# Performance work log

Hardware: AMD Instinct MI355X
Metric: run time of the kernel (lower is better)

The kernel has to match this reference:

```python
import jax, jax.numpy as jnp
import numpy as np

B = 4096
INPUT_SIZE = 1000
HIDDEN = 512
NUM_MASKS = 4
GROUP_SIZE = 100  # int(1000 * 0.1)
NUM_GROUPS = INPUT_SIZE // GROUP_SIZE  # 10, divides evenly


def entmax(alpha, v):
    # matches the torch helper: softmax-like with alpha-power denominator
    v = v - jnp.max(v, axis=-1, keepdims=True)
    e = jnp.exp(v)
    s = (jnp.sum(e ** alpha, axis=-1, keepdims=True) + 1e-5) ** (1.0 / alpha)
    return e / s


def layernorm(h, w, b):
    # h: [..., H]; w,b broadcast to [..., H]
    mu = jnp.mean(h, axis=-1, keepdims=True)
    var = jnp.mean((h - mu) ** 2, axis=-1, keepdims=True)
    return (h - mu) * jax.lax.rsqrt(var + 1e-5) * w + b


def setup_inputs() -> dict:
    key = jax.random.key(0)
    ks = jax.random.split(key, 4)
    x = jax.random.normal(ks[0], (B, INPUT_SIZE), dtype=jnp.float32)
    W_masks = jax.random.normal(ks[1], (NUM_GROUPS, NUM_MASKS, GROUP_SIZE), dtype=jnp.float32)
    W1 = jax.random.normal(ks[2], (NUM_GROUPS, HIDDEN, GROUP_SIZE), dtype=jnp.float32)
    W2 = jax.random.normal(ks[3], (NUM_GROUPS, HIDDEN, GROUP_SIZE), dtype=jnp.float32)
    ln1_w = jnp.ones((NUM_GROUPS, HIDDEN), dtype=jnp.float32)
    ln1_b = jnp.zeros((NUM_GROUPS, HIDDEN), dtype=jnp.float32)
    ln2_w = jnp.ones((NUM_GROUPS, HIDDEN), dtype=jnp.float32)
    ln2_b = jnp.zeros((NUM_GROUPS, HIDDEN), dtype=jnp.float32)
    return {"x": x, "W_masks": W_masks, "W1": W1, "W2": W2,
            "ln1_w": ln1_w, "ln1_b": ln1_b, "ln2_w": ln2_w, "ln2_b": ln2_b}


def reference(x, W_masks, W1, W2, ln1_w, ln1_b, ln2_w, ln2_b):
    G, M, S = W_masks.shape
    b = x.shape[0]
    xg = x.reshape(b, G, S)                                  # [B,G,S]
    mask = entmax(1.1, W_masks)                              # [G,M,S]
    weighted = xg[:, :, None, :] * mask[None]                # [B,G,M,S]
    h1 = jnp.einsum('bgms,ghs->bgmh', weighted, W1)          # [B,G,M,H]
    h2 = jnp.einsum('bgms,ghs->bgmh', weighted, W2)
    n1 = layernorm(h1, ln1_w[None, :, None, :], ln1_b[None, :, None, :])
    n2 = layernorm(h2, ln2_w[None, :, None, :], ln2_b[None, :, None, :])
    activated = jax.nn.relu(jax.nn.sigmoid(n1) * n2)         # [B,G,M,H]
    group_out = jnp.sum(activated, axis=2)                   # [B,G,H]
    return group_out.reshape(b, G * group_out.shape[-1])     # [B, G*H]
```

## Files before the change

kernel.cpp:

```cpp
#include <hip/hip_runtime.h>
#include <math.h>

typedef _Float16 half8 __attribute__((ext_vector_type(8)));
typedef float f32x4 __attribute__((ext_vector_type(4)));

namespace {
constexpr int BATCH = 4096;
constexpr int IN  = 1000;
constexpr int G   = 10;
constexpr int M   = 4;
constexpr int S   = 100;
constexpr int H   = 512;
constexpr int BB  = 16;
constexpr int R   = 64;
constexpr int NT  = 512;
constexpr int APITCH = 136;
constexpr int WPITCH = 40;
constexpr int WX_BYTES = R * APITCH * 2;
constexpr int WL_BYTES = 2 * H * WPITCH * 2;
}

__global__ __launch_bounds__(NT, 2)
void dfg_mfma_kernel(const float* __restrict__ x,
                     const float* __restrict__ Wm,
                     const float* __restrict__ W1,
                     const float* __restrict__ W2,
                     const float* __restrict__ ln1w,
                     const float* __restrict__ ln1b,
                     const float* __restrict__ ln2w,
                     const float* __restrict__ ln2b,
                     float* __restrict__ out) {
  __shared__ __align__(16) char smem[WX_BYTES + WL_BYTES];
  _Float16* wxs = (_Float16*)smem;
  _Float16* wl  = (_Float16*)(smem + WX_BYTES);
  float*    xs  = (float*)(smem + WX_BYTES);
  float*    msk = xs + BB * S;
  float4*   red = (float4*)smem;
  float4*   fin = (float4*)(smem + 64 * 9 * 16);

  const int tid = threadIdx.x;
  const int id      = blockIdx.x;
  const int logical = (id & 7) * 320 + (id >> 3);
  const int g  = logical >> 8;
  const int b0 = (logical & 255) * BB;

  const int wv = tid >> 6, l = tid & 63;
  const int lo = l & 15, hi = l >> 4;

  for (int f = tid; f < BB * 25; f += NT) {
    int bl = f / 25, s4 = f - bl * 25;
    *(float4*)&xs[bl * S + s4 * 4] =
        *(const float4*)(x + (size_t)(b0 + bl) * IN + g * S + s4 * 4);
  }
  if (wv < 4) {
    const float* wmp = Wm + (g * M + wv) * S;
    float v0 = (l < S) ? wmp[l] : -INFINITY;
    float v1 = (l + 64 < S) ? wmp[l + 64] : -INFINITY;
    float mx = fmaxf(v0, v1);
    #pragma unroll
    for (int d = 32; d >= 1; d >>= 1) mx = fmaxf(mx, __shfl_xor(mx, d));
    float e0 = (l < S) ? expf(v0 - mx) : 0.f;
    float e1 = (l + 64 < S) ? expf(v1 - mx) : 0.f;
    float a0 = (l < S) ? expf(1.1f * (v0 - mx)) : 0.f;
    float a1 = (l + 64 < S) ? expf(1.1f * (v1 - mx)) : 0.f;
    float ss = a0 + a1;
    #pragma unroll
    for (int d = 32; d >= 1; d >>= 1) ss += __shfl_xor(ss, d);
    float inv = 1.0f / powf(ss + 1e-5f, 1.0f / 1.1f);
    if (l < S) msk[wv * S + l] = e0 * inv;
    if (l + 64 < S) msk[wv * S + l + 64] = e1 * inv;
  }
  __syncthreads();

  {
    const int r = tid & 63;
    const int c = tid >> 6;
    const int bl = r & 15, m = r >> 4;
    const int sBeg = c * 13;
    const int sEnd = (sBeg + 13 < S) ? sBeg + 13 : S;
    for (int s = sBeg; s < sEnd; ++s)
      wxs[r * APITCH + s] = (_Float16)(xs[bl * S + s] * msk[m * S + s]);
  }
  for (int f = tid; f < R * 14; f += NT) {
    int r = f / 14, j = f - r * 14;
    *(unsigned int*)&wxs[r * APITCH + 100 + j * 2] = 0u;
  }
  __syncthreads();

  f32x4 acc1[4][4] = {};
  f32x4 acc2[4][4] = {};
  const float* W1g = W1 + (size_t)g * H * S;
  const float* W2g = W2 + (size_t)g * H * S;

  #pragma unroll
  for (int ks = 0; ks < 4; ++ks) {
    #pragma unroll
    for (int mat = 0; mat < 2; ++mat) {
      const float* Wg = mat ? W2g : W1g;
      #pragma unroll
      for (int i = 0; i < 8; ++i) {
        int f = tid + i * NT;
        int h = f >> 3, s4 = f & 7;
        union { _Float16 hh[4]; unsigned int u[2]; } pk;
        if (ks < 3 || s4 == 0) {
          float4 v = *(const float4*)(Wg + h * S + ks * 32 + s4 * 4);
          pk.hh[0] = (_Float16)v.x; pk.hh[1] = (_Float16)v.y;
          pk.hh[2] = (_Float16)v.z; pk.hh[3] = (_Float16)v.w;
        } else { pk.u[0] = 0u; pk.u[1] = 0u; }
        *(uint2*)&wl[mat * H * WPITCH + h * WPITCH + s4 * 4] = *(uint2*)pk.u;
      }
    }
    __syncthreads();

    half8 xf[4];
    #pragma unroll
    for (int rt = 0; rt < 4; ++rt)
      xf[rt] = *(const half8*)&wxs[(rt * 16 + lo) * APITCH + ks * 32 + 8 * hi];
    #pragma unroll
    for (int ht = 0; ht < 4; ++ht) {
      const int hrow = 64 * wv + ht * 16 + lo;
      half8 wf1 = *(const half8*)&wl[hrow * WPITCH + 8 * hi];
      half8 wf2 = *(const half8*)&wl[H * WPITCH + hrow * WPITCH + 8 * hi];
      #pragma unroll
      for (int rt = 0; rt < 4; ++rt) {
        acc1[ht][rt] = __builtin_amdgcn_mfma_f32_16x16x32_f16(wf1, xf[rt], acc1[ht][rt], 0, 0, 0);
        acc2[ht][rt] = __builtin_amdgcn_mfma_f32_16x16x32_f16(wf2, xf[rt], acc2[ht][rt], 0, 0, 0);
      }
    }
    __syncthreads();
  }

  float st1[4], sq1[4], st2[4], sq2[4];
  #pragma unroll
  for (int rt = 0; rt < 4; ++rt) {
    float s1 = 0.f, q1 = 0.f, s2 = 0.f, q2 = 0.f;
    #pragma unroll
    for (int ht = 0; ht < 4; ++ht)
      #pragma unroll
      for (int rg = 0; rg < 4; ++rg) {
        float a = acc1[ht][rt][rg], b = acc2[ht][rt][rg];
        s1 += a; q1 += a * a; s2 += b; q2 += b * b;
      }
    st1[rt] = s1; sq1[rt] = q1; st2[rt] = s2; sq2[rt] = q2;
  }
  #pragma unroll
  for (int d = 16; d <= 32; d <<= 1) {
    #pragma unroll
    for (int rt = 0; rt < 4; ++rt) {
      st1[rt] += __shfl_xor(st1[rt], d); sq1[rt] += __shfl_xor(sq1[rt], d);
      st2[rt] += __shfl_xor(st2[rt], d); sq2[rt] += __shfl_xor(sq2[rt], d);
    }
  }
  if (hi == 0) {
    #pragma unroll
    for (int rt = 0; rt < 4; ++rt)
      red[(rt * 16 + lo) * 9 + wv] = make_float4(st1[rt], sq1[rt], st2[rt], sq2[rt]);
  }
  __syncthreads();
  if (tid < 64) {
    float4 t = make_float4(0.f, 0.f, 0.f, 0.f);
    #pragma unroll
    for (int j = 0; j < 8; ++j) {
      float4 v = red[tid * 9 + j];
      t.x += v.x; t.y += v.y; t.z += v.z; t.w += v.w;
    }
    float mu1 = t.x * (1.f / H), mu2 = t.z * (1.f / H);
    float va = t.y * (1.f / H) - mu1 * mu1;
    float vb = t.w * (1.f / H) - mu2 * mu2;
    fin[tid] = make_float4(mu1, rsqrtf(va + 1e-5f), mu2, rsqrtf(vb + 1e-5f));
  }
  __syncthreads();

  float4 fr[4];
  #pragma unroll
  for (int rt = 0; rt < 4; ++rt) fr[rt] = fin[rt * 16 + lo];
  const float* p1w = ln1w + g * H; const float* p1b = ln1b + g * H;
  const float* p2w = ln2w + g * H; const float* p2b = ln2b + g * H;
  float* orow = out + (size_t)(b0 + lo) * (G * H) + g * H;
  #pragma unroll
  for (int ht = 0; ht < 4; ++ht) {
    const int hb = 64 * wv + ht * 16 + 4 * hi;
    float4 w1v = *(const float4*)(p1w + hb);
    float4 b1v = *(const float4*)(p1b + hb);
    float4 w2v = *(const float4*)(p2w + hb);
    float4 b2v = *(const float4*)(p2b + hb);
    float o[4] = {0.f, 0.f, 0.f, 0.f};
    #pragma unroll
    for (int rt = 0; rt < 4; ++rt) {
      #pragma unroll
      for (int rg = 0; rg < 4; ++rg) {
        float n1 = (acc1[ht][rt][rg] - fr[rt].x) * fr[rt].y * (&w1v.x)[rg] + (&b1v.x)[rg];
        float n2 = (acc2[ht][rt][rg] - fr[rt].z) * fr[rt].w * (&w2v.x)[rg] + (&b2v.x)[rg];
        float sg = 1.0f / (1.0f + __expf(-n1));
        o[rg] += fmaxf(sg * n2, 0.f);
      }
    }
    *(float4*)(orow + hb) = make_float4(o[0], o[1], o[2], o[3]);
  }
}

extern "C" void kernel_launch(void* const* d_in, const int* in_sizes, int n_in,
                              void* d_out, int out_size, void* d_ws, size_t ws_size,
                              hipStream_t stream) {
  const float* x   = (const float*)d_in[0];
  const float* Wm  = (const float*)d_in[1];
  const float* W1  = (const float*)d_in[2];
  const float* W2  = (const float*)d_in[3];
  const float* l1w = (const float*)d_in[4];
  const float* l1b = (const float*)d_in[5];
  const float* l2w = (const float*)d_in[6];
  const float* l2b = (const float*)d_in[7];
  float* outp = (float*)d_out;
  dfg_mfma_kernel<<<(BATCH / BB) * G, NT, 0, stream>>>(
      x, Wm, W1, W2, l1w, l1b, l2w, l2b, outp);
}
```

Measured before the change: 297.9 us.

## Pre-convert weights to padded fp16 and load MFMA fragments directly from global

Adds a pre-pass kernel that converts W1/W2 to fp16 with K padded to 128 in workspace. The main kernel then reads weight fragments straight from global memory into registers instead of staging them through LDS, which removes the per-k-step LDS writes and barriers. It also vectorizes the masked-x build with 16-byte LDS stores. In exchange there is an extra kernel launch each call and the weight reads now rely on cache hits rather than LDS reuse. If no workspace is available, it falls back to converting fp32 weights in registers.

```diff
diff --git a/kernel.cpp b/kernel.cpp
--- a/kernel.cpp
+++ b/kernel.cpp
@@ -14,29 +14,59 @@
 constexpr int BB  = 16;
 constexpr int R   = 64;
 constexpr int NT  = 512;
-constexpr int APITCH = 136;
-constexpr int WPITCH = 40;
-constexpr int WX_BYTES = R * APITCH * 2;
-constexpr int WL_BYTES = 2 * H * WPITCH * 2;
-}
-
+constexpr int KP  = 128;
+constexpr int WXP = 136;
+constexpr int OFF_XS  = R * WXP * 2;
+constexpr int OFF_MSK = OFF_XS + BB * S * 4;
+constexpr int LDS_SZ  = OFF_MSK + M * S * 4;
+constexpr int OFF_FIN = 64 * 9 * 16;
+constexpr size_t WMAT = (size_t)G * H * KP;
+constexpr size_t W16_BYTES = 2 * WMAT * sizeof(_Float16);
+}
+
+__global__ __launch_bounds__(256)
+void cvt_w_kernel(const float* __restrict__ W1, const float* __restrict__ W2,
+                  _Float16* __restrict__ w16) {
+  const int t = blockIdx.x * 256 + threadIdx.x;
+  const int c = t & 15;
+  const int row = t >> 4;
+  const int mat = row / (G * H);
+  const int r2  = row - mat * (G * H);
+  const float* src = (mat ? W2 : W1) + (size_t)r2 * S;
+  union { _Float16 h[8]; uint4 u; } o;
+  #pragma unroll
+  for (int j = 0; j < 8; ++j) {
+    const int k = c * 8 + j;
+    o.h[j] = (k < S) ? (_Float16)src[k] : (_Float16)0.f;
+  }
+  *(uint4*)&w16[(size_t)row * KP + c * 8] = o.u;
+}
+
+__device__ inline half8 pk8(float4 a, float4 b) {
+  half8 r;
+  r[0] = (_Float16)a.x; r[1] = (_Float16)a.y; r[2] = (_Float16)a.z; r[3] = (_Float16)a.w;
+  r[4] = (_Float16)b.x; r[5] = (_Float16)b.y; r[6] = (_Float16)b.z; r[7] = (_Float16)b.w;
+  return r;
+}
+
+template <bool PRE>
 __global__ __launch_bounds__(NT, 2)
-void dfg_mfma_kernel(const float* __restrict__ x,
-                     const float* __restrict__ Wm,
-                     const float* __restrict__ W1,
-                     const float* __restrict__ W2,
-                     const float* __restrict__ ln1w,
-                     const float* __restrict__ ln1b,
-                     const float* __restrict__ ln2w,
-                     const float* __restrict__ ln2b,
-                     float* __restrict__ out) {
-  __shared__ __align__(16) char smem[WX_BYTES + WL_BYTES];
+void dfg_mfma3_kernel(const float* __restrict__ x,
+                      const float* __restrict__ Wm,
+                      const _Float16* __restrict__ w16,
+                      const float* __restrict__ W1f,
+                      const float* __restrict__ W2f,
+                      const float* __restrict__ ln1w,
+                      const float* __restrict__ ln1b,
+                      const float* __restrict__ ln2w,
+                      const float* __restrict__ ln2b,
+                      float* __restrict__ out) {
+  __shared__ __align__(16) char smem[LDS_SZ];
   _Float16* wxs = (_Float16*)smem;
-  _Float16* wl  = (_Float16*)(smem + WX_BYTES);
-  float*    xs  = (float*)(smem + WX_BYTES);
-  float*    msk = xs + BB * S;
+  float*    xs  = (float*)(smem + OFF_XS);
+  float*    msk = (float*)(smem + OFF_MSK);
   float4*   red = (float4*)smem;
-  float4*   fin = (float4*)(smem + 64 * 9 * 16);
+  float4*   fin = (float4*)(smem + OFF_FIN);
 
   const int tid = threadIdx.x;
   const int id      = blockIdx.x;
@@ -73,62 +103,65 @@
   __syncthreads();
 
   {
-    const int r = tid & 63;
-    const int c = tid >> 6;
+    const int r = tid >> 3;
+    const int j = tid & 7;
     const int bl = r & 15, m = r >> 4;
-    const int sBeg = c * 13;
-    const int sEnd = (sBeg + 13 < S) ? sBeg + 13 : S;
-    for (int s = sBeg; s < sEnd; ++s)
-      wxs[r * APITCH + s] = (_Float16)(xs[bl * S + s] * msk[m * S + s]);
-  }
-  for (int f = tid; f < R * 14; f += NT) {
-    int r = f / 14, j = f - r * 14;
-    *(unsigned int*)&wxs[r * APITCH + 100 + j * 2] = 0u;
+    union { _Float16 h[16]; uint4 u[2]; } o;
+    #pragma unroll
+    for (int i = 0; i < 16; ++i) {
+      const int k = j * 16 + i;
+      float v = 0.f;
+      if (k < S) v = xs[bl * S + k] * msk[m * S + k];
+      o.h[i] = (_Float16)v;
+    }
+    *(uint4*)&wxs[r * WXP + j * 16]     = o.u[0];
+    *(uint4*)&wxs[r * WXP + j * 16 + 8] = o.u[1];
   }
   __syncthreads();
 
   f32x4 acc1[4][4] = {};
   f32x4 acc2[4][4] = {};
-  const float* W1g = W1 + (size_t)g * H * S;
-  const float* W2g = W2 + (size_t)g * H * S;
+  const _Float16* w1p = PRE ? w16 + (size_t)g * H * KP : nullptr;
+  const _Float16* w2p = PRE ? w1p + WMAT : nullptr;
+  const float* W1g = W1f + (size_t)g * H * S;
+  const float* W2g = W2f + (size_t)g * H * S;
 
   #pragma unroll
   for (int ks = 0; ks < 4; ++ks) {
-    #pragma unroll
-    for (int mat = 0; mat < 2; ++mat) {
-      const float* Wg = mat ? W2g : W1g;
-      #pragma unroll
-      for (int i = 0; i < 8; ++i) {
-        int f = tid + i * NT;
-        int h = f >> 3, s4 = f & 7;
-        union { _Float16 hh[4]; unsigned int u[2]; } pk;
-        if (ks < 3 || s4 == 0) {
-          float4 v = *(const float4*)(Wg + h * S + ks * 32 + s4 * 4);
-          pk.hh[0] = (_Float16)v.x; pk.hh[1] = (_Float16)v.y;
-          pk.hh[2] = (_Float16)v.z; pk.hh[3] = (_Float16)v.w;
-        } else { pk.u[0] = 0u; pk.u[1] = 0u; }
-        *(uint2*)&wl[mat * H * WPITCH + h * WPITCH + s4 * 4] = *(uint2*)pk.u;
-      }
-    }
-    __syncthreads();
-
     half8 xf[4];
     #pragma unroll
     for (int rt = 0; rt < 4; ++rt)
-      xf[rt] = *(const half8*)&wxs[(rt * 16 + lo) * APITCH + ks * 32 + 8 * hi];
+      xf[rt] = *(const half8*)&wxs[(rt * 16 + lo) * WXP + ks * 32 + 8 * hi];
     #pragma unroll
     for (int ht = 0; ht < 4; ++ht) {
       const int hrow = 64 * wv + ht * 16 + lo;
-      half8 wf1 = *(const half8*)&wl[hrow * WPITCH + 8 * hi];
-      half8 wf2 = *(const half8*)&wl[H * WPITCH + hrow * WPITCH + 8 * hi];
+      half8 wf1, wf2;
+      if constexpr (PRE) {
+        wf1 = *(const half8*)&w1p[(size_t)hrow * KP + ks * 32 + 8 * hi];
+        wf2 = *(const half8*)&w2p[(size_t)hrow * KP + ks * 32 + 8 * hi];
+      } else {
+        const float* s1 = W1g + (size_t)hrow * S + ks * 32 + 8 * hi;
+        const float* s2 = W2g + (size_t)hrow * S + ks * 32 + 8 * hi;
+        if (ks < 3) {
+          wf1 = pk8(*(const float4*)s1, *(const float4*)(s1 + 4));
+          wf2 = pk8(*(const float4*)s2, *(const float4*)(s2 + 4));
+        } else if (hi == 0) {
+          float4 z = make_float4(0.f, 0.f, 0.f, 0.f);
+          wf1 = pk8(*(const float4*)s1, z);
+          wf2 = pk8(*(const float4*)s2, z);
+        } else {
+          half8 zz = {};
+          wf1 = zz; wf2 = zz;
+        }
+      }
       #pragma unroll
       for (int rt = 0; rt < 4; ++rt) {
         acc1[ht][rt] = __builtin_amdgcn_mfma_f32_16x16x32_f16(wf1, xf[rt], acc1[ht][rt], 0, 0, 0);
         acc2[ht][rt] = __builtin_amdgcn_mfma_f32_16x16x32_f16(wf2, xf[rt], acc2[ht][rt], 0, 0, 0);
       }
     }
-    __syncthreads();
-  }
+  }
+  __syncthreads();
 
   float st1[4], sq1[4], st2[4], sq2[4];
   #pragma unroll
@@ -211,6 +244,16 @@
   const float* l2w = (const float*)d_in[6];
   const float* l2b = (const float*)d_in[7];
   float* outp = (float*)d_out;
-  dfg_mfma_kernel<<<(BATCH / BB) * G, NT, 0, stream>>>(
-      x, Wm, W1, W2, l1w, l1b, l2w, l2b, outp);
-}
+
+  const dim3 grid((BATCH / BB) * G);
+  if (ws_size >= W16_BYTES && d_ws != nullptr) {
+    _Float16* w16 = (_Float16*)d_ws;
+    const int cvt_threads = 2 * G * H * (KP / 8);
+    cvt_w_kernel<<<cvt_threads / 256, 256, 0, stream>>>(W1, W2, w16);
+    dfg_mfma3_kernel<true><<<grid, NT, 0, stream>>>(
+        x, Wm, w16, W1, W2, l1w, l1b, l2w, l2b, outp);
+  } else {
+    dfg_mfma3_kernel<false><<<grid, NT, 0, stream>>>(
+        x, Wm, nullptr, W1, W2, l1w, l1b, l2w, l2b, outp);
+  }
+}
```

After: 285.5 us. -4.2%, faster.
